# Optimization experiments

Measured on AMD Instinct MI355X. Metric: run time of the kernel, lower is better.

## Reference

```python
import jax, jax.numpy as jnp
import numpy as np

N_NODES = 50000
N_EDGES = 800000
NUM_FEATURES = 128
HIDDEN = 128


def _gcn_conv(x, src, dst, norm, W, b, num_nodes):
    # x: [N, F_in], W: [F_in, F_out]
    h = x @ W                              # dense transform first (PyG order)
    msg = h[src] * norm[:, None]           # gather + per-edge scale
    out = jax.ops.segment_sum(msg, dst, num_segments=num_nodes)  # scatter-add
    return out + b


def _prep_edges(edge_index, num_nodes):
    # add self loops
    loop = jnp.arange(num_nodes, dtype=edge_index.dtype)
    src = jnp.concatenate([edge_index[0], loop])
    dst = jnp.concatenate([edge_index[1], loop])
    # symmetric normalization deg^{-1/2}[src] * deg^{-1/2}[dst]
    deg = jax.ops.segment_sum(jnp.ones_like(dst, dtype=jnp.float32), dst,
                              num_segments=num_nodes)
    dinv = jnp.where(deg > 0, jax.lax.rsqrt(deg), 0.0)
    norm = dinv[src] * dinv[dst]
    return src, dst, norm


def setup_inputs() -> dict:
    key = jax.random.key(0)
    ks = jax.random.split(key, 5)
    s1 = 1.0 / np.sqrt(NUM_FEATURES)
    s2 = 1.0 / np.sqrt(HIDDEN)
    return {
        "x": jax.random.normal(ks[0], (N_NODES, NUM_FEATURES), jnp.float32),
        "edge_index": jax.random.randint(ks[1], (2, N_EDGES), 0, N_NODES,
                                         dtype=jnp.int64),
        "W1": jax.random.normal(ks[2], (NUM_FEATURES, HIDDEN), jnp.float32) * s1,
        "b1": jnp.zeros((HIDDEN,), jnp.float32),
        "W2": jax.random.normal(ks[3], (HIDDEN, HIDDEN), jnp.float32) * s2,
        "b2": jnp.zeros((HIDDEN,), jnp.float32),
        "Wout": jax.random.normal(ks[4], (HIDDEN, 1), jnp.float32) * s2,
        "bout": jnp.zeros((1,), jnp.float32),
    }


def reference(x, edge_index, W1, b1, W2, b2, Wout, bout):
    num_nodes = x.shape[0]
    src, dst, norm = _prep_edges(edge_index, num_nodes)
    h = _gcn_conv(x, src, dst, norm, W1, b1, num_nodes)
    h = jax.nn.relu(h)
    h = _gcn_conv(h, src, dst, norm, W2, b2, num_nodes)
    h = jax.nn.relu(h)
    return jax.nn.sigmoid(h @ Wout + bout)
```

## Files before the change

### kernel.cpp

```cpp
#include <hip/hip_runtime.h>
#include <math.h>

#define NN 50000
#define NE 800000
#define NBUK 196
#define PBLK 256
#define EPB (NE / PBLK)

typedef __attribute__((ext_vector_type(8))) short bf16x8;
typedef __attribute__((ext_vector_type(4))) float f32x4;

__device__ __forceinline__ unsigned short f2b(float f) {
  union { float f; unsigned u; } v; v.f = f;
  unsigned r = v.u + 0x7FFF + ((v.u >> 16) & 1);
  return (unsigned short)(r >> 16);
}
__device__ __forceinline__ float plo(unsigned v) {
  union { unsigned u; float f; } t; t.u = v << 16; return t.f;
}
__device__ __forceinline__ float phi(unsigned v) {
  union { unsigned u; float f; } t; t.u = v & 0xFFFF0000u; return t.f;
}

__device__ __forceinline__ int edge_val(const void* ei, long long idx, int is64) {
  if (is64) return (int)((const long long*)ei)[idx];
  return ((const int*)ei)[idx];
}

__global__ __launch_bounds__(256) void k_phist(const void* __restrict__ ei,
                                               int* __restrict__ bh,
                                               const float* __restrict__ W1,
                                               const float* __restrict__ W2,
                                               unsigned short* __restrict__ Wt1,
                                               unsigned short* __restrict__ Wt2) {
  if (threadIdx.x < 128) {
    int gi = blockIdx.x * 128 + threadIdx.x;
    int sel = gi >> 14;
    int j = gi & 16383;
    int k = j >> 7, n = j & 127;
    (sel ? Wt2 : Wt1)[n * 128 + k] = f2b((sel ? W2 : W1)[j]);
  }
  __shared__ int hist[NBUK];
  __shared__ int sflag;
  if (threadIdx.x < 64) {
    unsigned v = ((const unsigned*)ei)[2 * threadIdx.x + 1];
    unsigned long long m = __ballot(v == 0u);
    if (threadIdx.x == 0) sflag = (m == ~0ull) ? 1 : 0;
  }
  if (threadIdx.x < NBUK) hist[threadIdx.x] = 0;
  __syncthreads();
  int is64 = sflag;
  int base = blockIdx.x * EPB;
  for (int e = base + threadIdx.x; e < base + EPB; e += 256) {
    int d = edge_val(ei, (long long)NE + e, is64);
    atomicAdd(&hist[d >> 8], 1);
  }
  __syncthreads();
  if (threadIdx.x < NBUK) bh[threadIdx.x * PBLK + blockIdx.x] = hist[threadIdx.x];
}

__global__ __launch_bounds__(256) void k_pscanA(int* __restrict__ bh,
                                                int* __restrict__ colsum) {
  __shared__ int sh[256];
  int k = blockIdx.x, t = threadIdx.x;
  int v = bh[k * PBLK + t];
  sh[t] = v;
  __syncthreads();
  for (int s = 1; s < 256; s <<= 1) {
    int u = (t >= s) ? sh[t - s] : 0;
    __syncthreads();
    sh[t] += u;
    __syncthreads();
  }
  bh[k * PBLK + t] = sh[t] - v;
  if (t == 255) colsum[k] = sh[255];
}

__global__ __launch_bounds__(256) void k_pscanB(const int* __restrict__ colsum,
                                                int* __restrict__ bstart) {
  __shared__ int sh[256];
  int t = threadIdx.x;
  sh[t] = (t < NBUK) ? colsum[t] : 0;
  __syncthreads();
  for (int s = 1; s < 256; s <<= 1) {
    int u = (t >= s) ? sh[t - s] : 0;
    __syncthreads();
    sh[t] += u;
    __syncthreads();
  }
  if (t <= NBUK) bstart[t] = (t == 0) ? 0 : sh[t - 1];
}

__global__ __launch_bounds__(256) void k_pscat(const void* __restrict__ ei,
                                               const int* __restrict__ bh,
                                               const int* __restrict__ bstart,
                                               unsigned* __restrict__ epk) {
  __shared__ int cur[NBUK];
  __shared__ int sflag;
  if (threadIdx.x < 64) {
    unsigned v = ((const unsigned*)ei)[2 * threadIdx.x + 1];
    unsigned long long m = __ballot(v == 0u);
    if (threadIdx.x == 0) sflag = (m == ~0ull) ? 1 : 0;
  }
  if (threadIdx.x < NBUK)
    cur[threadIdx.x] = bstart[threadIdx.x] + bh[threadIdx.x * PBLK + blockIdx.x];
  __syncthreads();
  int is64 = sflag;
  int base = blockIdx.x * EPB;
  for (int e = base + threadIdx.x; e < base + EPB; e += 256) {
    int d = edge_val(ei, (long long)NE + e, is64);
    int s = edge_val(ei, e, is64);
    int p = atomicAdd(&cur[d >> 8], 1);
    epk[p] = (unsigned)s | ((unsigned)(d & 255) << 16);
  }
}

__global__ __launch_bounds__(256) void k_bofffill(const unsigned* __restrict__ epk,
                                                  const int* __restrict__ bstart,
                                                  int* __restrict__ off,
                                                  float* __restrict__ dinv,
                                                  unsigned short* __restrict__ csr16) {
  __shared__ int hist[256];
  __shared__ int cur[256];
  int k = blockIdx.x, t = threadIdx.x;
  hist[t] = 0;
  __syncthreads();
  int e0 = bstart[k], e1 = bstart[k + 1];
  for (int e = e0 + t; e < e1; e += 256)
    atomicAdd(&hist[(epk[e] >> 16) & 255], 1);
  __syncthreads();
  int myc = hist[t];
  for (int s = 1; s < 256; s <<= 1) {
    int u = (t >= s) ? hist[t - s] : 0;
    __syncthreads();
    hist[t] += u;
    __syncthreads();
  }
  int excl = hist[t] - myc;
  int node = k * 256 + t;
  if (node < NN) {
    off[node] = e0 + excl;
    dinv[node] = rsqrtf((float)(myc + 1));
  }
  cur[t] = e0 + excl;
  __syncthreads();
  for (int e = e0 + t; e < e1; e += 256) {
    unsigned pk = epk[e];
    int p = atomicAdd(&cur[(pk >> 16) & 255], 1);
    csr16[p] = (unsigned short)(pk & 0xFFFFu);
  }
  if (k == 0 && t == 0) off[NN] = NE;
}

template <int A_F32>
__global__ __launch_bounds__(256, 2) void k_mgemm(const void* __restrict__ Ap,
                                                  const unsigned short* __restrict__ Wt,
                                                  const float* __restrict__ dinv,
                                                  unsigned short* __restrict__ Out,
                                                  int M) {
  int wid  = (blockIdx.x * blockDim.x + threadIdx.x) >> 6;
  int lane = threadIdx.x & 63;
  int nw   = (gridDim.x * blockDim.x) >> 6;
  int r  = lane & 15;
  int kg = lane >> 4;
  bf16x8 wf[8][4];
#pragma unroll
  for (int n = 0; n < 8; ++n)
#pragma unroll
    for (int kk = 0; kk < 4; ++kk)
      wf[n][kk] = *(const bf16x8*)&Wt[(n * 16 + r) * 128 + kk * 32 + kg * 8];
  int nstr = M >> 4;
  for (int s = wid; s < nstr; s += nw) {
    int row = s * 16 + r;
    bf16x8 xf[4];
    if (A_F32) {
      const float* Ar = (const float*)Ap + (long long)row * 128 + kg * 8;
#pragma unroll
      for (int kk = 0; kk < 4; ++kk) {
        float4 lo4 = *(const float4*)(Ar + kk * 32);
        float4 hi4 = *(const float4*)(Ar + kk * 32 + 4);
        bf16x8 t;
        t[0] = (short)f2b(lo4.x); t[1] = (short)f2b(lo4.y);
        t[2] = (short)f2b(lo4.z); t[3] = (short)f2b(lo4.w);
        t[4] = (short)f2b(hi4.x); t[5] = (short)f2b(hi4.y);
        t[6] = (short)f2b(hi4.z); t[7] = (short)f2b(hi4.w);
        xf[kk] = t;
      }
    } else {
      const unsigned short* Ar = (const unsigned short*)Ap;
#pragma unroll
      for (int kk = 0; kk < 4; ++kk)
        xf[kk] = *(const bf16x8*)(Ar + ((size_t)(kk * NN + row) * 32) + kg * 8);
    }
    f32x4 acc[8];
#pragma unroll
    for (int n = 0; n < 8; ++n) acc[n] = (f32x4){0.f, 0.f, 0.f, 0.f};
#pragma unroll
    for (int kk = 0; kk < 4; ++kk)
#pragma unroll
      for (int n = 0; n < 8; ++n)
        acc[n] = __builtin_amdgcn_mfma_f32_16x16x32_bf16(wf[n][kk], xf[kk], acc[n], 0, 0, 0);
    float dv = dinv[row];
#pragma unroll
    for (int n = 0; n < 8; ++n) {
      int q = n >> 1;
      unsigned short* Or = Out + ((size_t)(q * NN + row) * 32) + (n & 1) * 16 + kg * 4;
      uint2 o;
      o.x = (unsigned)f2b(acc[n][0] * dv) | ((unsigned)f2b(acc[n][1] * dv) << 16);
      o.y = (unsigned)f2b(acc[n][2] * dv) | ((unsigned)f2b(acc[n][3] * dv) << 16);
      *(uint2*)Or = o;
    }
  }
}

template <int FINAL>
__global__ __launch_bounds__(256) void k_agg(const unsigned short* __restrict__ Tb,
                                             const int* __restrict__ off,
                                             const unsigned short* __restrict__ csr16,
                                             const float* __restrict__ dinv,
                                             const float* __restrict__ bias,
                                             const float* __restrict__ wout,
                                             void* __restrict__ outp) {
  const unsigned* Tw = (const unsigned*)Tb;
  int bid  = blockIdx.x;
  int xcd  = bid & 7;
  int q    = xcd >> 1;
  int wb   = (bid >> 3) * 2 + (xcd & 1);
  int wave = threadIdx.x >> 6;
  int lane = threadIdx.x & 63;
  int slot = lane >> 4;
  int li   = lane & 15;
  int gw   = wb * 4 + wave;
  float2 bb = ((const float2*)bias)[q * 16 + li];
  float2 ww = make_float2(0.f, 0.f);
  if (FINAL) ww = ((const float2*)wout)[q * 16 + li];
  const size_t qbase = (size_t)q * NN;
  for (int d0 = gw * 4; d0 < NN; d0 += 8192) {
    int d = d0 + slot;
    int e0 = off[d], e1 = off[d + 1];
    unsigned v = Tw[(qbase + d) * 16 + li];
    float a0 = plo(v), a1 = phi(v);
    int e = e0;
    for (; e + 4 <= e1; e += 4) {
      int sA = csr16[e];
      int sB = csr16[e + 1];
      int sC = csr16[e + 2];
      int sD = csr16[e + 3];
      unsigned vA = Tw[(qbase + sA) * 16 + li];
      unsigned vB = Tw[(qbase + sB) * 16 + li];
      unsigned vC = Tw[(qbase + sC) * 16 + li];
      unsigned vD = Tw[(qbase + sD) * 16 + li];
      a0 += plo(vA); a1 += phi(vA);
      a0 += plo(vB); a1 += phi(vB);
      a0 += plo(vC); a1 += phi(vC);
      a0 += plo(vD); a1 += phi(vD);
    }
    for (; e < e1; ++e) {
      int sA = csr16[e];
      unsigned vA = Tw[(qbase + sA) * 16 + li];
      a0 += plo(vA); a1 += phi(vA);
    }
    float dv = dinv[d];
    a0 = fmaxf(fmaf(a0, dv, bb.x), 0.f);
    a1 = fmaxf(fmaf(a1, dv, bb.y), 0.f);
    if (FINAL) {
      float r = a0 * ww.x + a1 * ww.y;
      r += __shfl_xor(r, 1, 64);
      r += __shfl_xor(r, 2, 64);
      r += __shfl_xor(r, 4, 64);
      r += __shfl_xor(r, 8, 64);
      if (li == 0) ((float*)outp)[qbase + d] = r;
    } else {
      ((unsigned*)outp)[(qbase + d) * 16 + li] =
          (unsigned)f2b(a0) | ((unsigned)f2b(a1) << 16);
    }
  }
}

__global__ __launch_bounds__(256) void k_fin(const float* __restrict__ part,
                                             const float* __restrict__ bout,
                                             float* __restrict__ out) {
  int i = blockIdx.x * 256 + threadIdx.x;
  if (i >= NN) return;
  float r = part[i] + part[NN + i] + part[2 * NN + i] + part[3 * NN + i] + bout[0];
  out[i] = 1.f / (1.f + __expf(-r));
}

extern "C" void kernel_launch(void* const* d_in, const int* in_sizes, int n_in,
                              void* d_out, int out_size, void* d_ws, size_t ws_size,
                              hipStream_t stream) {
  const float* x  = (const float*)d_in[0];
  const void*  ei = d_in[1];
  const float* W1 = (const float*)d_in[2];
  const float* b1 = (const float*)d_in[3];
  const float* W2 = (const float*)d_in[4];
  const float* b2 = (const float*)d_in[5];
  const float* Wo = (const float*)d_in[6];
  const float* bo = (const float*)d_in[7];
  float* out = (float*)d_out;

  char* p = (char*)d_ws;
  auto alloc = [&](size_t bytes) {
    char* r = p;
    p += (bytes + 511) & ~(size_t)511;
    return r;
  };
  int*   bh     = (int*)alloc(sizeof(int) * NBUK * PBLK);
  int*   colsum = (int*)alloc(sizeof(int) * NBUK);
  int*   bstart = (int*)alloc(sizeof(int) * (NBUK + 1));
  int*   off    = (int*)alloc(sizeof(int) * (NN + 1));
  float* dinv   = (float*)alloc(sizeof(float) * NN);
  unsigned short* csr16 = (unsigned short*)alloc(sizeof(short) * NE);
  unsigned short* Wt1 = (unsigned short*)alloc(sizeof(short) * 128 * 128);
  unsigned short* Wt2 = (unsigned short*)alloc(sizeof(short) * 128 * 128);
  unsigned short* T   = (unsigned short*)alloc(sizeof(short) * (size_t)NN * 128);
  unsigned short* H   = (unsigned short*)alloc(sizeof(short) * (size_t)NN * 128);
  float* part = (float*)alloc(sizeof(float) * 4 * NN);
  unsigned* epk = (unsigned*)T;

  k_phist<<<PBLK, 256, 0, stream>>>(ei, bh, W1, W2, Wt1, Wt2);
  k_pscanA<<<NBUK, 256, 0, stream>>>(bh, colsum);
  k_pscanB<<<1, 256, 0, stream>>>(colsum, bstart);
  k_pscat<<<PBLK, 256, 0, stream>>>(ei, bh, bstart, epk);
  k_bofffill<<<NBUK, 256, 0, stream>>>(epk, bstart, off, dinv, csr16);

  k_mgemm<1><<<512, 256, 0, stream>>>(x, Wt1, dinv, T, NN);
  k_agg<0><<<2048, 256, 0, stream>>>(T, off, csr16, dinv, b1, nullptr, H);
  k_mgemm<0><<<512, 256, 0, stream>>>(H, Wt2, dinv, T, NN);
  k_agg<1><<<2048, 256, 0, stream>>>(T, off, csr16, dinv, b2, Wo, part);
  k_fin<<<(NN + 255) / 256, 256, 0, stream>>>(part, bo, out);
}
```

Baseline: 217.9 us.

## Fold bucket scan into scatter kernels and fuse final layer output into aggregation

Removes the single-block bucket-start scan kernel by having each scatter and fill block rescan the small column-sum array in shared memory. Replaces the second aggregation plus the sigmoid kernel with one kernel that gives each node a full wave. The wave splits that node's edges across four lane groups, each gathering 16-byte chunks covering all 128 features. It then reduces across groups and features with shuffles and writes the sigmoid output directly. This cuts two launches and the partial-sum buffer, at the cost of redundant per-block scans and a different work mapping for aggregation.

```diff
diff --git a/kernel.cpp b/kernel.cpp
--- a/kernel.cpp
+++ b/kernel.cpp
@@ -76,9 +76,8 @@
   if (t == 255) colsum[k] = sh[255];
 }
 
-__global__ __launch_bounds__(256) void k_pscanB(const int* __restrict__ colsum,
-                                                int* __restrict__ bstart) {
-  __shared__ int sh[256];
+__device__ __forceinline__ void scan_colsum(const int* __restrict__ colsum,
+                                            int* sh) {
   int t = threadIdx.x;
   sh[t] = (t < NBUK) ? colsum[t] : 0;
   __syncthreads();
@@ -88,13 +87,13 @@
     sh[t] += u;
     __syncthreads();
   }
-  if (t <= NBUK) bstart[t] = (t == 0) ? 0 : sh[t - 1];
 }
 
 __global__ __launch_bounds__(256) void k_pscat(const void* __restrict__ ei,
                                                const int* __restrict__ bh,
-                                               const int* __restrict__ bstart,
+                                               const int* __restrict__ colsum,
                                                unsigned* __restrict__ epk) {
+  __shared__ int bs[256];
   __shared__ int cur[NBUK];
   __shared__ int sflag;
   if (threadIdx.x < 64) {
@@ -102,8 +101,11 @@
     unsigned long long m = __ballot(v == 0u);
     if (threadIdx.x == 0) sflag = (m == ~0ull) ? 1 : 0;
   }
-  if (threadIdx.x < NBUK)
-    cur[threadIdx.x] = bstart[threadIdx.x] + bh[threadIdx.x * PBLK + blockIdx.x];
+  scan_colsum(colsum, bs);
+  if (threadIdx.x < NBUK) {
+    int bstart = (threadIdx.x == 0) ? 0 : bs[threadIdx.x - 1];
+    cur[threadIdx.x] = bstart + bh[threadIdx.x * PBLK + blockIdx.x];
+  }
   __syncthreads();
   int is64 = sflag;
   int base = blockIdx.x * EPB;
@@ -116,16 +118,19 @@
 }
 
 __global__ __launch_bounds__(256) void k_bofffill(const unsigned* __restrict__ epk,
-                                                  const int* __restrict__ bstart,
+                                                  const int* __restrict__ colsum,
                                                   int* __restrict__ off,
                                                   float* __restrict__ dinv,
                                                   unsigned short* __restrict__ csr16) {
+  __shared__ int bs[256];
   __shared__ int hist[256];
   __shared__ int cur[256];
   int k = blockIdx.x, t = threadIdx.x;
+  scan_colsum(colsum, bs);
+  int e0 = (k == 0) ? 0 : bs[k - 1];
+  int e1 = bs[k];
   hist[t] = 0;
   __syncthreads();
-  int e0 = bstart[k], e1 = bstart[k + 1];
   for (int e = e0 + t; e < e1; e += 256)
     atomicAdd(&hist[(epk[e] >> 16) & 255], 1);
   __syncthreads();
@@ -213,14 +218,12 @@
   }
 }
 
-template <int FINAL>
-__global__ __launch_bounds__(256) void k_agg(const unsigned short* __restrict__ Tb,
-                                             const int* __restrict__ off,
-                                             const unsigned short* __restrict__ csr16,
-                                             const float* __restrict__ dinv,
-                                             const float* __restrict__ bias,
-                                             const float* __restrict__ wout,
-                                             void* __restrict__ outp) {
+__global__ __launch_bounds__(256) void k_agg0(const unsigned short* __restrict__ Tb,
+                                              const int* __restrict__ off,
+                                              const unsigned short* __restrict__ csr16,
+                                              const float* __restrict__ dinv,
+                                              const float* __restrict__ bias,
+                                              unsigned* __restrict__ outp) {
   const unsigned* Tw = (const unsigned*)Tb;
   int bid  = blockIdx.x;
   int xcd  = bid & 7;
@@ -232,8 +235,6 @@
   int li   = lane & 15;
   int gw   = wb * 4 + wave;
   float2 bb = ((const float2*)bias)[q * 16 + li];
-  float2 ww = make_float2(0.f, 0.f);
-  if (FINAL) ww = ((const float2*)wout)[q * 16 + li];
   const size_t qbase = (size_t)q * NN;
   for (int d0 = gw * 4; d0 < NN; d0 += 8192) {
     int d = d0 + slot;
@@ -263,27 +264,74 @@
     float dv = dinv[d];
     a0 = fmaxf(fmaf(a0, dv, bb.x), 0.f);
     a1 = fmaxf(fmaf(a1, dv, bb.y), 0.f);
-    if (FINAL) {
-      float r = a0 * ww.x + a1 * ww.y;
-      r += __shfl_xor(r, 1, 64);
-      r += __shfl_xor(r, 2, 64);
-      r += __shfl_xor(r, 4, 64);
-      r += __shfl_xor(r, 8, 64);
-      if (li == 0) ((float*)outp)[qbase + d] = r;
-    } else {
-      ((unsigned*)outp)[(qbase + d) * 16 + li] =
-          (unsigned)f2b(a0) | ((unsigned)f2b(a1) << 16);
-    }
-  }
-}
-
-__global__ __launch_bounds__(256) void k_fin(const float* __restrict__ part,
-                                             const float* __restrict__ bout,
-                                             float* __restrict__ out) {
-  int i = blockIdx.x * 256 + threadIdx.x;
-  if (i >= NN) return;
-  float r = part[i] + part[NN + i] + part[2 * NN + i] + part[3 * NN + i] + bout[0];
-  out[i] = 1.f / (1.f + __expf(-r));
+    outp[(qbase + d) * 16 + li] = (unsigned)f2b(a0) | ((unsigned)f2b(a1) << 16);
+  }
+}
+
+__global__ __launch_bounds__(256) void k_agg1(const unsigned short* __restrict__ Tb,
+                                              const int* __restrict__ off,
+                                              const unsigned short* __restrict__ csr16,
+                                              const float* __restrict__ dinv,
+                                              const float* __restrict__ bias,
+                                              const float* __restrict__ wout,
+                                              const float* __restrict__ bout,
+                                              float* __restrict__ out) {
+  const uint4* Tw4 = (const uint4*)Tb;
+  int wid  = (blockIdx.x * blockDim.x + threadIdx.x) >> 6;
+  int nw   = (gridDim.x * blockDim.x) >> 6;
+  int lane = threadIdx.x & 63;
+  int grp  = lane >> 4;
+  int li   = lane & 15;
+  int q    = li >> 2;
+  int w    = li & 3;
+  float4 bA = ((const float4*)bias)[q * 8 + w * 2];
+  float4 bB = ((const float4*)bias)[q * 8 + w * 2 + 1];
+  float4 wA = ((const float4*)wout)[q * 8 + w * 2];
+  float4 wB = ((const float4*)wout)[q * 8 + w * 2 + 1];
+  const size_t qbase = (size_t)q * NN;
+  for (int d = wid; d < NN; d += nw) {
+    int e0 = off[d], e1 = off[d + 1];
+    int ne = e1 - e0;
+    int np = ne >> 2, rem = ne & 3;
+    int s_init = (grp == 0) ? d : ((grp - 1) < rem ? (int)csr16[e1 - 1 - (grp - 1)] : -1);
+    float a0 = 0.f, a1 = 0.f, a2 = 0.f, a3 = 0.f, a4 = 0.f, a5 = 0.f, a6 = 0.f, a7 = 0.f;
+    if (s_init >= 0) {
+      uint4 v = Tw4[(qbase + s_init) * 4 + w];
+      a0 = plo(v.x); a1 = phi(v.x); a2 = plo(v.y); a3 = phi(v.y);
+      a4 = plo(v.z); a5 = phi(v.z); a6 = plo(v.w); a7 = phi(v.w);
+    }
+    int base = e0 + grp;
+    for (int st = 0; st < np; ++st) {
+      int s = csr16[base + 4 * st];
+      uint4 v = Tw4[(qbase + s) * 4 + w];
+      a0 += plo(v.x); a1 += phi(v.x); a2 += plo(v.y); a3 += phi(v.y);
+      a4 += plo(v.z); a5 += phi(v.z); a6 += plo(v.w); a7 += phi(v.w);
+    }
+    a0 += __shfl_xor(a0, 16, 64); a1 += __shfl_xor(a1, 16, 64);
+    a2 += __shfl_xor(a2, 16, 64); a3 += __shfl_xor(a3, 16, 64);
+    a4 += __shfl_xor(a4, 16, 64); a5 += __shfl_xor(a5, 16, 64);
+    a6 += __shfl_xor(a6, 16, 64); a7 += __shfl_xor(a7, 16, 64);
+    a0 += __shfl_xor(a0, 32, 64); a1 += __shfl_xor(a1, 32, 64);
+    a2 += __shfl_xor(a2, 32, 64); a3 += __shfl_xor(a3, 32, 64);
+    a4 += __shfl_xor(a4, 32, 64); a5 += __shfl_xor(a5, 32, 64);
+    a6 += __shfl_xor(a6, 32, 64); a7 += __shfl_xor(a7, 32, 64);
+    float dv = dinv[d];
+    a0 = fmaxf(fmaf(a0, dv, bA.x), 0.f);
+    a1 = fmaxf(fmaf(a1, dv, bA.y), 0.f);
+    a2 = fmaxf(fmaf(a2, dv, bA.z), 0.f);
+    a3 = fmaxf(fmaf(a3, dv, bA.w), 0.f);
+    a4 = fmaxf(fmaf(a4, dv, bB.x), 0.f);
+    a5 = fmaxf(fmaf(a5, dv, bB.y), 0.f);
+    a6 = fmaxf(fmaf(a6, dv, bB.z), 0.f);
+    a7 = fmaxf(fmaf(a7, dv, bB.w), 0.f);
+    float r = a0 * wA.x + a1 * wA.y + a2 * wA.z + a3 * wA.w
+            + a4 * wB.x + a5 * wB.y + a6 * wB.z + a7 * wB.w;
+    r += __shfl_xor(r, 8, 64);
+    r += __shfl_xor(r, 4, 64);
+    r += __shfl_xor(r, 2, 64);
+    r += __shfl_xor(r, 1, 64);
+    if (lane == 0) out[d] = 1.f / (1.f + __expf(-(r + bout[0])));
+  }
 }
 
 extern "C" void kernel_launch(void* const* d_in, const int* in_sizes, int n_in,
@@ -307,7 +355,6 @@
   };
   int*   bh     = (int*)alloc(sizeof(int) * NBUK * PBLK);
   int*   colsum = (int*)alloc(sizeof(int) * NBUK);
-  int*   bstart = (int*)alloc(sizeof(int) * (NBUK + 1));
   int*   off    = (int*)alloc(sizeof(int) * (NN + 1));
   float* dinv   = (float*)alloc(sizeof(float) * NN);
   unsigned short* csr16 = (unsigned short*)alloc(sizeof(short) * NE);
@@ -315,18 +362,15 @@
   unsigned short* Wt2 = (unsigned short*)alloc(sizeof(short) * 128 * 128);
   unsigned short* T   = (unsigned short*)alloc(sizeof(short) * (size_t)NN * 128);
   unsigned short* H   = (unsigned short*)alloc(sizeof(short) * (size_t)NN * 128);
-  float* part = (float*)alloc(sizeof(float) * 4 * NN);
   unsigned* epk = (unsigned*)T;
 
   k_phist<<<PBLK, 256, 0, stream>>>(ei, bh, W1, W2, Wt1, Wt2);
   k_pscanA<<<NBUK, 256, 0, stream>>>(bh, colsum);
-  k_pscanB<<<1, 256, 0, stream>>>(colsum, bstart);
-  k_pscat<<<PBLK, 256, 0, stream>>>(ei, bh, bstart, epk);
-  k_bofffill<<<NBUK, 256, 0, stream>>>(epk, bstart, off, dinv, csr16);
+  k_pscat<<<PBLK, 256, 0, stream>>>(ei, bh, colsum, epk);
+  k_bofffill<<<NBUK, 256, 0, stream>>>(epk, colsum, off, dinv, csr16);
 
   k_mgemm<1><<<512, 256, 0, stream>>>(x, Wt1, dinv, T, NN);
-  k_agg<0><<<2048, 256, 0, stream>>>(T, off, csr16, dinv, b1, nullptr, H);
+  k_agg0<<<2048, 256, 0, stream>>>(T, off, csr16, dinv, b1, (unsigned*)H);
   k_mgemm<0><<<512, 256, 0, stream>>>(H, Wt2, dinv, T, NN);
-  k_agg<1><<<2048, 256, 0, stream>>>(T, off, csr16, dinv, b2, Wo, part);
-  k_fin<<<(NN + 255) / 256, 256, 0, stream>>>(part, bo, out);
-}
+  k_agg1<<<2048, 256, 0, stream>>>(T, off, csr16, dinv, b2, Wo, bo, out);
+}
```

Result: slower. 226.3 us (+3.8%).
